# Performance work log

Measured on AMD Instinct MI355X. Metric: run time of the kernel, lower is better.

The kernel has to match this reference:

```python
import jax, jax.numpy as jnp
import numpy as np

B, TP, TF = 256, 128, 64
COV, D, OUT, CTRL, H, L = 64, 64, 32, 128, 512, 2


def _gru_layer(x, Wih, Whh, bih, bhh):
    # x: [B, T, in]; torch GRU gate order: r, z, n
    xg = jnp.einsum('bti,gi->btg', x, Wih) + bih  # [B, T, 3H]
    h0 = jnp.zeros((x.shape[0], Whh.shape[1]), x.dtype)

    def step(h, xg_t):
        gh = h @ Whh.T + bhh
        xr, xz, xn = jnp.split(xg_t, 3, axis=-1)
        hr, hz, hn = jnp.split(gh, 3, axis=-1)
        r = jax.nn.sigmoid(xr + hr)
        z = jax.nn.sigmoid(xz + hz)
        n = jnp.tanh(xn + r * hn)
        h = (1.0 - z) * n + z * h
        return h, h

    _, hs = jax.lax.scan(step, h0, jnp.swapaxes(xg, 0, 1))
    return jnp.swapaxes(hs, 0, 1)  # [B, T, H]


def setup_inputs() -> dict:
    key = jax.random.key(0)
    ks = jax.random.split(key, 32)
    s = 0.05
    inp = {
        'past_input': jax.random.normal(ks[0], (B, TP, COV), jnp.float32),
        'past_label': jax.random.normal(ks[1], (B, TP, OUT), jnp.float32),
        'future_input': jax.random.normal(ks[2], (B, TF, COV), jnp.float32),
        'gru_Wih_0': s * jax.random.normal(ks[3], (3 * H, COV), jnp.float32),
        'gru_Whh_0': s * jax.random.normal(ks[4], (3 * H, H), jnp.float32),
        'gru_bih_0': s * jax.random.normal(ks[5], (3 * H,), jnp.float32),
        'gru_bhh_0': s * jax.random.normal(ks[6], (3 * H,), jnp.float32),
        'gru_Wih_1': s * jax.random.normal(ks[7], (3 * H, H), jnp.float32),
        'gru_Whh_1': s * jax.random.normal(ks[8], (3 * H, H), jnp.float32),
        'gru_bih_1': s * jax.random.normal(ks[9], (3 * H,), jnp.float32),
        'gru_bhh_1': s * jax.random.normal(ks[10], (3 * H,), jnp.float32),
        'flow_u': s * jax.random.normal(ks[11], (D,), jnp.float32),
        'flow_w': s * jax.random.normal(ks[12], (D,), jnp.float32),
        'flow_b': s * jax.random.normal(ks[13], (D,), jnp.float32),
        'feat_W': s * jax.random.normal(ks[14], (D, H), jnp.float32),
        'feat_b': s * jax.random.normal(ks[15], (D,), jnp.float32),
        'ctrl_W1': s * jax.random.normal(ks[16], (CTRL, OUT), jnp.float32),
        'ctrl_b1': s * jax.random.normal(ks[17], (CTRL,), jnp.float32),
        'ctrl_W2': s * jax.random.normal(ks[18], (2 * D, CTRL), jnp.float32),
        'ctrl_b2': s * jax.random.normal(ks[19], (2 * D,), jnp.float32),
        'ctrlmu_W': s * jax.random.normal(ks[20], (D, D), jnp.float32),
        'ctrlmu_b': s * jax.random.normal(ks[21], (D,), jnp.float32),
        'out_W': s * jax.random.normal(ks[22], (OUT, D), jnp.float32),
        'out_b': s * jax.random.normal(ks[23], (OUT,), jnp.float32),
    }
    return inp


def reference(past_input, past_label, future_input,
              gru_Wih_0, gru_Whh_0, gru_bih_0, gru_bhh_0,
              gru_Wih_1, gru_Whh_1, gru_bih_1, gru_bhh_1,
              flow_u, flow_w, flow_b, feat_W, feat_b,
              ctrl_W1, ctrl_b1, ctrl_W2, ctrl_b2,
              ctrlmu_W, ctrlmu_b, out_W, out_b):
    cov = jnp.concatenate([past_input, future_input], axis=1)  # [B, T, COV]
    h1 = _gru_layer(cov, gru_Wih_0, gru_Whh_0, gru_bih_0, gru_bhh_0)
    cov_feat = _gru_layer(h1, gru_Wih_1, gru_Whh_1, gru_bih_1, gru_bhh_1)  # [B, T, H]
    Tp = past_input.shape[1]
    bsz = past_input.shape[0]

    def trans(mu_past, var_past, cov_t):
        # per-dim PlanarFlow vectorized over transition_dim
        a = jnp.tanh(flow_w * mu_past + flow_b)
        mu_prior = flow_u * a + cov_t @ feat_W.T + feat_b + mu_past
        coef = flow_u * flow_w * (1.0 - a * a)
        var_prior = 2.0 * coef * var_past + var_past + 1.0
        return mu_prior, var_prior

    def control(ctrl_in, mu_prior):
        hdn = jnp.tanh(ctrl_in @ ctrl_W1.T + ctrl_b1)
        cm, cls = jnp.split(hdn @ ctrl_W2.T + ctrl_b2, 2, axis=-1)
        cm = cm - (mu_prior @ ctrlmu_W.T + ctrlmu_b)
        return cm, jax.nn.softplus(cls)

    def fuse(mu_pr, var_pr, mu_po, var_po):
        s = var_po + var_pr
        mu_w = (var_po / s) * mu_pr + (var_pr / s) * mu_po
        return mu_w, var_pr * var_po / s

    def past_step(carry, xs):
        mu_post, var_post = carry
        cov_t, lab_t = xs
        mu_pr, var_pr = trans(mu_post, var_post, cov_t)
        pred = mu_pr @ out_W.T + out_b
        cm, cs = control(lab_t, mu_pr)
        return fuse(mu_pr, var_pr, cm, cs), (pred, cm, cs)

    def fut_step(carry, cov_t):
        mu_post, var_post = carry
        mu_pr, var_pr = trans(mu_post, var_post, cov_t)
        pred = mu_pr @ out_W.T + out_b
        cm, cs = control(pred, mu_pr)
        return fuse(mu_pr, var_pr, cm, cs), (pred, cm, cs)

    init = (jnp.zeros((bsz, D), cov.dtype), jnp.ones((bsz, D), cov.dtype))
    cov_p = jnp.swapaxes(cov_feat[:, :Tp], 0, 1)
    lab_p = jnp.swapaxes(past_label, 0, 1)
    carry, (pp, cmp_, csp) = jax.lax.scan(past_step, init, (cov_p, lab_p))
    cov_f = jnp.swapaxes(cov_feat[:, Tp:], 0, 1)
    _, (pf, cmf, csf) = jax.lax.scan(fut_step, carry, cov_f)

    pred = jnp.swapaxes(jnp.concatenate([pp, pf], axis=0), 0, 1)        # [B, T, OUT]
    cm = jnp.swapaxes(jnp.concatenate([cmp_, cmf], axis=0), 0, 1)[:, 1:]  # [B, T-1, D]
    cs = jnp.swapaxes(jnp.concatenate([csp, csf], axis=0), 0, 1)[:, 1:]   # [B, T-1, D]
    return pred, cm, cs
```

## Files before the change

### kernel.cpp

```cpp
#include <hip/hip_runtime.h>
#include <stdint.h>

#define DEV static __device__ __forceinline__

using short8 = __attribute__((ext_vector_type(8))) short;
using f32x4  = __attribute__((ext_vector_type(4))) float;
using gbl_u32 = const __attribute__((address_space(1))) unsigned int;
using lds_u32 = __attribute__((address_space(3))) unsigned int;

DEV float bf2f(short s) {
  unsigned u = ((unsigned)(unsigned short)s) << 16;
  float f; __builtin_memcpy(&f, &u, 4); return f;
}
DEV short f2bf(float f) {
  unsigned u; __builtin_memcpy(&u, &f, 4);
  u = (u + 0x7fffu + ((u >> 16) & 1u)) >> 16;
  return (short)u;
}
DEV void gload_lds16(const void* g, void* l) {
  __builtin_amdgcn_global_load_lds((gbl_u32*)g, (lds_u32*)l, 16, 0, 0);
}
DEV float sigm(float x) { return 1.f / (1.f + __expf(-x)); }
DEV float tanh_f(float x) {
  float e = __expf(2.f * x);
  return 1.f - 2.f * __builtin_amdgcn_rcpf(e + 1.f);
}
DEV unsigned load_agent(const unsigned int* p) {
  return __hip_atomic_load(p, __ATOMIC_RELAXED, __HIP_MEMORY_SCOPE_AGENT);
}
DEV void bar() {
  asm volatile("s_waitcnt lgkmcnt(0)" ::: "memory");
  __builtin_amdgcn_sched_barrier(0);
  __builtin_amdgcn_s_barrier();
  __builtin_amdgcn_sched_barrier(0);
}

__global__ void pack_covf_k(const float* __restrict__ past, const float* __restrict__ fut,
                            short* __restrict__ covf) {
  const int n = 192 * 16 * 2 * 512;
  for (int i = blockIdx.x * blockDim.x + threadIdx.x; i < n; i += gridDim.x * blockDim.x) {
    int e = i & 7, l = (i >> 3) & 63, kf = (i >> 9) & 1, g = (i >> 10) & 15, t = i >> 14;
    int b = g * 16 + (l & 15);
    int col = kf * 32 + (l >> 4) * 8 + e;
    float v = (t < 128) ? past[((size_t)b * 128 + t) * 64 + col]
                        : fut[((size_t)b * 64 + (t - 128)) * 64 + col];
    covf[i] = f2bf(v);
  }
}

__global__ void pack_lab_k(const float* __restrict__ lab, short* __restrict__ labp) {
  const int n = 128 * 256 * 32;
  for (int i = blockIdx.x * blockDim.x + threadIdx.x; i < n; i += gridDim.x * blockDim.x) {
    int c = i & 31, r = i >> 5;
    int b = r & 255, t = r >> 8;
    labp[i] = f2bf(lab[((size_t)b * 128 + t) * 32 + c]);
  }
}

DEV int gru_srcrow(int pr) {
  int j = pr / 96, w = pr % 96;
  return ((w >> 5) << 9) + j * 32 + (w & 31);
}

__global__ void pack_gru_k(const float* __restrict__ Wih, const float* __restrict__ Whh,
                           const float* __restrict__ bih, const float* __restrict__ bhh,
                           int Kin, short* __restrict__ Wihp, short* __restrict__ Whhp,
                           float* __restrict__ bihp, float* __restrict__ bhhp) {
  const int nW1 = 1536 * Kin, nW2 = 1536 * 512;
  const int total = nW1 + nW2 + 3072;
  for (int idx = blockIdx.x * blockDim.x + threadIdx.x; idx < total; idx += gridDim.x * blockDim.x) {
    if (idx < nW1) {
      int pr = idx / Kin, k = idx - pr * Kin;
      Wihp[idx] = f2bf(Wih[(size_t)gru_srcrow(pr) * Kin + k]);
    } else if (idx < nW1 + nW2) {
      int ii = idx - nW1;
      int j = ii / 49152, r = ii - j * 49152;
      int i = r & 7, slot = r >> 3;
      int l = slot & 63, sf = slot >> 6;
      int kqg = sf / 6, tile = sf - kqg * 6;
      int w = tile * 16 + (l & 15);
      int k = kqg * 32 + (l >> 4) * 8 + i;
      int srow = (w >> 5) * 512 + j * 32 + (w & 31);
      Whhp[ii] = f2bf(Whh[(size_t)srow * 512 + k]);
    } else if (idx < nW1 + nW2 + 1536) {
      int pr = idx - nW1 - nW2;
      bihp[pr] = bih[gru_srcrow(pr)];
    } else {
      int pr = idx - nW1 - nW2 - 1536;
      bhhp[pr] = bhh[gru_srcrow(pr)];
    }
  }
}

__global__ void pack_wih0f_k(const float* __restrict__ Wih0, short* __restrict__ wf) {
  const int n = 16 * 6 * 2 * 512;
  for (int i = blockIdx.x * blockDim.x + threadIdx.x; i < n; i += gridDim.x * blockDim.x) {
    int j = i / 6144, r = i - j * 6144;
    int tile = r >> 10, kf = (r >> 9) & 1, l = (r >> 3) & 63, e = r & 7;
    int srow = gru_srcrow(j * 96 + tile * 16 + (l & 15));
    int k = kf * 32 + (l >> 4) * 8 + e;
    wf[i] = f2bf(Wih0[(size_t)srow * 64 + k]);
  }
}

__global__ void pack_misc_k(const float* __restrict__ fw, const float* __restrict__ w1,
                            const float* __restrict__ w2, short* __restrict__ fwb,
                            short* __restrict__ w1b, short* __restrict__ w2b) {
  const int n1 = 64 * 512, n2 = 128 * 32, n3 = 128 * 128;
  const int total = n1 + n2 + n3;
  for (int i = blockIdx.x * blockDim.x + threadIdx.x; i < total; i += gridDim.x * blockDim.x) {
    if (i < n1) fwb[i] = f2bf(fw[i]);
    else if (i < n1 + n2) w1b[i - n1] = f2bf(w1[i - n1]);
    else w2b[i - n1 - n2] = f2bf(w2[i - n1 - n2]);
  }
}

__global__ void pack_vae_k(const float* __restrict__ outW, const float* __restrict__ cmuW,
                           const float* __restrict__ W1, const float* __restrict__ W2,
                           short* __restrict__ vwf) {
  const int n = 52 * 512;
  for (int i = blockIdx.x * blockDim.x + threadIdx.x; i < n; i += gridDim.x * blockDim.x) {
    int fr = i >> 9, l = (i >> 3) & 63, e = i & 7;
    int lm = l & 15, lh = l >> 4;
    float v;
    if (fr < 4) { int kt = fr >> 1, nt = fr & 1; v = outW[(nt * 16 + lm) * 64 + kt * 32 + lh * 8 + e]; }
    else if (fr < 12) { int f = fr - 4, kt = f >> 2, nt = f & 3; v = cmuW[(nt * 16 + lm) * 64 + kt * 32 + lh * 8 + e]; }
    else if (fr < 20) { int nt = fr - 12; v = W1[(nt * 16 + lm) * 32 + lh * 8 + e]; }
    else { int f = fr - 20, kt = f >> 3, nt = f & 7; v = W2[(nt * 16 + lm) * 128 + kt * 32 + lh * 8 + e]; }
    vwf[i] = f2bf(v);
  }
}

template <int BK, bool OBF16, bool DOTANH, bool AFRAG, int CMODE = 0>
__global__ __launch_bounds__(256) void gemm_bt_k(
    const short* __restrict__ A, const short* __restrict__ Bw,
    const float* __restrict__ bias, void* __restrict__ Cout,
    int M, int N, int K) {
  constexpr int BM = 128, BN = 128;
  __shared__ short As[BM * BK];
  __shared__ short Bs[BN * BK];
  const int tid = threadIdx.x, lane = tid & 63;
  const int wave = tid >> 6, wm = wave >> 1, wn = wave & 1;
  const int bm = blockIdx.x, bn = blockIdx.y;
  const int lm = lane & 15, lk = (lane >> 4) * 8;
  f32x4 acc[4][4] = {};
  for (int k0 = 0; k0 < K; k0 += BK) {
    constexpr int BYTES = BM * BK * 2;
#pragma unroll
    for (int it = 0; it < BYTES / 4096; ++it) {
      int o = it * 4096 + tid * 16;
      if (AFRAG) {
        int sub = o >> 10, gl = sub >> 1, kk2 = sub & 1, inb = o & 1023;
        size_t region = ((size_t)(bm >> 1) * 16 + (bm & 1) * 8 + gl) * 16 + (k0 >> 5) + kk2;
        gload_lds16((const char*)A + region * 1024 + inb, (char*)As + (o - lane * 16));
      } else {
        int row = o / (BK * 2);
        int col = o - row * (BK * 2);
        const char* srcA = (const char*)A + (((size_t)(bm * BM + row)) * K + k0) * 2 + col;
        gload_lds16(srcA, (char*)As + (o - lane * 16));
      }
      int row = o / (BK * 2);
      int col = o - row * (BK * 2);
      int rb = bn * BN + row;
      if (rb >= N) rb = N - 1;
      const char* srcB = (const char*)Bw + (((size_t)rb) * K + k0) * 2 + col;
      gload_lds16(srcB, (char*)Bs + (o - lane * 16));
    }
    __syncthreads();
#pragma unroll
    for (int kk = 0; kk < BK / 32; ++kk) {
      short8 av[4], bv[4];
#pragma unroll
      for (int i = 0; i < 4; ++i) {
        if (AFRAG)
          av[i] = *(const short8*)((const char*)As + (((wm * 4 + i) * 2 + kk) << 10) + lane * 16);
        else
          av[i] = *(const short8*)((const char*)As + ((wm * 64 + i * 16 + lm) * BK + kk * 32 + lk) * 2);
      }
#pragma unroll
      for (int jv = 0; jv < 4; ++jv)
        bv[jv] = *(const short8*)((const char*)Bs + ((wn * 64 + jv * 16 + lm) * BK + kk * 32 + lk) * 2);
#pragma unroll
      for (int i = 0; i < 4; ++i)
#pragma unroll
        for (int jv = 0; jv < 4; ++jv)
          acc[i][jv] = __builtin_amdgcn_mfma_f32_16x16x32_bf16(av[i], bv[jv], acc[i][jv], 0, 0, 0);
    }
    __syncthreads();
  }
  if (CMODE == 1) {
    const int NT = N >> 4;
#pragma unroll
    for (int jv = 0; jv < 4; ++jv) {
      int col = bn * BN + wn * 64 + jv * 16 + lm;
      if (col >= N) continue;
      float bvl = bias[col];
#pragma unroll
      for (int i = 0; i < 4; ++i) {
        int rowblk = bm * 8 + wm * 4 + i;
        f32x4 v = acc[i][jv];
        v[0] += bvl; v[1] += bvl; v[2] += bvl; v[3] += bvl;
        *(f32x4*)((float*)Cout + (((size_t)rowblk * NT + (col >> 4)) << 8) + lane * 4) = v;
      }
    }
  } else {
#pragma unroll
    for (int jv = 0; jv < 4; ++jv) {
      int col = bn * BN + wn * 64 + jv * 16 + lm;
      if (col >= N) continue;
      float bvl = bias[col];
#pragma unroll
      for (int i = 0; i < 4; ++i) {
        int row0 = bm * BM + wm * 64 + i * 16 + (lane >> 4) * 4;
#pragma unroll
        for (int r = 0; r < 4; ++r) {
          float v = acc[i][jv][r] + bvl;
          if (DOTANH) v = tanhf(v);
          size_t off = (size_t)(row0 + r) * N + col;
          if (OBF16) ((short*)Cout)[off] = f2bf(v);
          else ((float*)Cout)[off] = v;
        }
      }
    }
  }
}

template <int XGF>
__global__ __launch_bounds__(256) void gru_scan_k(
    const short* __restrict__ xg,
    const short* __restrict__ covf,
    const short* __restrict__ wihf_g,
    const short* __restrict__ Whhp,
    const float* __restrict__ bihp,
    const float* __restrict__ bhhp,
    short* __restrict__ hbuf,
    unsigned int* __restrict__ flags,
    int t0, int nsteps) {
  __shared__ short Wl[96 * 512];
  __shared__ short hs[16 * 512];
  __shared__ float sc[2][16 * 101];
  __shared__ float scx[2][16 * 33];
  __shared__ float bhs[96];
  __shared__ float bihn[32];
  const int tid = threadIdx.x, lane = tid & 63, wave = tid >> 6;
  const int x = blockIdx.x;
  const int g = (x & 7) + ((x >> 7) << 3);
  const int j = (x >> 3) & 15;
  unsigned int* __restrict__ myflags = flags + g * 16;
  unsigned int* __restrict__ hbuf32 = (unsigned int*)hbuf;
  {
    const char* wsrc = (const char*)Whhp + (size_t)j * 98304;
#pragma unroll 4
    for (int it = 0; it < 24; ++it) {
      int o = it * 4096 + tid * 16;
      gload_lds16(wsrc + o, (char*)Wl + (o - lane * 16));
    }
    if (tid < 96) {
      float b = bhhp[j * 96 + tid];
      if (XGF && tid < 64) b += bihp[j * 96 + tid];
      bhs[tid] = b;
    }
    if (XGF && tid < 32) bihn[tid] = bihp[j * 96 + 64 + tid];
  }
  const int wk = wave >> 1, wn3 = wave & 1;
  const int m = tid >> 4, up = tid & 15, u0 = up * 2;
  short8 wihf0{}, wihf1{}, wihf2{};
  if (XGF) {
    wihf0 = *(const short8*)(wihf_g + ((size_t)(j * 6 + wn3 * 3 + 0) * 2 + wk) * 512 + lane * 8);
    wihf1 = *(const short8*)(wihf_g + ((size_t)(j * 6 + wn3 * 3 + 1) * 2 + wk) * 512 + lane * 8);
    wihf2 = *(const short8*)(wihf_g + ((size_t)(j * 6 + wn3 * 3 + 2) * 2 + wk) * 512 + lane * 8);
  }
  for (int tl = 0; tl < nsteps; ++tl) {
    const int t = t0 + tl;
    if (tl > 0) {
      const unsigned tgt = (unsigned)tl;
      if (tid < 16) {
        const unsigned int* fp = myflags + tid;
        int guard = 0;
        while (load_agent(fp) < tgt && ++guard < 400000) {}
      }
    }
    __syncthreads();
    const char* hsrc = (const char*)hbuf + ((size_t)t * 16 + g) * 16384;
#pragma unroll
    for (int it = 0; it < 4; ++it) {
      int o = it * 4096 + tid * 16;
      gload_lds16(hsrc + o, (char*)hs + (o - lane * 16));
    }
    short8 cf{};
    unsigned int xr2 = 0, xz2 = 0, xn2 = 0;
    if (XGF) {
      cf = *(const short8*)(covf + (((size_t)t * 16 + g) * 2 + wk) * 512 + lane * 8);
    } else {
      const unsigned int* xp = (const unsigned int*)(xg + ((size_t)tl * 256 + g * 16 + m) * 1536 + j * 96);
      xr2 = xp[up]; xz2 = xp[16 + up]; xn2 = xp[32 + up];
    }
    __syncthreads();
    f32x4 a3[3] = {};
    f32x4 ax0 = {0.f, 0.f, 0.f, 0.f}, ax1 = {0.f, 0.f, 0.f, 0.f};
#pragma unroll
    for (int kq = 0; kq < 8; ++kq) {
      int kqg = wk * 8 + kq;
      short8 av = *(const short8*)((const char*)hs + (kqg << 10) + lane * 16);
#pragma unroll
      for (int n = 0; n < 3; ++n) {
        short8 bv = *(const short8*)((const char*)Wl + ((kqg * 6 + wn3 * 3 + n) << 10) + lane * 16);
        a3[n] = __builtin_amdgcn_mfma_f32_16x16x32_bf16(av, bv, a3[n], 0, 0, 0);
      }
    }
    if (XGF) {
      a3[0] = __builtin_amdgcn_mfma_f32_16x16x32_bf16(cf, wihf0, a3[0], 0, 0, 0);
      if (wn3 == 0) {
        a3[1] = __builtin_amdgcn_mfma_f32_16x16x32_bf16(cf, wihf1, a3[1], 0, 0, 0);
        a3[2] = __builtin_amdgcn_mfma_f32_16x16x32_bf16(cf, wihf2, a3[2], 0, 0, 0);
      } else {
        ax0 = __builtin_amdgcn_mfma_f32_16x16x32_bf16(cf, wihf1, ax0, 0, 0, 0);
        ax1 = __builtin_amdgcn_mfma_f32_16x16x32_bf16(cf, wihf2, ax1, 0, 0, 0);
      }
    }
#pragma unroll
    for (int n = 0; n < 3; ++n)
#pragma unroll
      for (int rr = 0; rr < 4; ++rr)
        sc[wk][((lane >> 4) * 4 + rr) * 101 + (wn3 * 3 + n) * 16 + (lane & 15)] = a3[n][rr];
    if (XGF && wn3 == 1) {
#pragma unroll
      for (int rr = 0; rr < 4; ++rr) {
        scx[wk][((lane >> 4) * 4 + rr) * 33 + (lane & 15)] = ax0[rr];
        scx[wk][((lane >> 4) * 4 + rr) * 33 + 16 + (lane & 15)] = ax1[rr];
      }
    }
    __syncthreads();
    {
      float Sr0 = sc[0][m * 101 + u0] + sc[1][m * 101 + u0];
      float Sr1 = sc[0][m * 101 + u0 + 1] + sc[1][m * 101 + u0 + 1];
      float Sz0 = sc[0][m * 101 + 32 + u0] + sc[1][m * 101 + 32 + u0];
      float Sz1 = sc[0][m * 101 + 33 + u0] + sc[1][m * 101 + 33 + u0];
      float Sn0 = sc[0][m * 101 + 64 + u0] + sc[1][m * 101 + 64 + u0];
      float Sn1 = sc[0][m * 101 + 65 + u0] + sc[1][m * 101 + 65 + u0];
      int hpa = ((j * 64 + (up >> 2) * 16 + m) << 4) + ((u0 & 7) << 1);
      unsigned int hpu = *(const unsigned int*)((const char*)hs + hpa);
      float hp0 = bf2f((short)(hpu & 0xffff)), hp1 = bf2f((short)(hpu >> 16));
      float r0, r1, z0, z1, n0, n1;
      if (XGF) {
        float Sx0 = scx[0][m * 33 + u0] + scx[1][m * 33 + u0];
        float Sx1 = scx[0][m * 33 + u0 + 1] + scx[1][m * 33 + u0 + 1];
        r0 = sigm(Sr0 + bhs[u0]);
        r1 = sigm(Sr1 + bhs[u0 + 1]);
        z0 = sigm(Sz0 + bhs[32 + u0]);
        z1 = sigm(Sz1 + bhs[33 + u0]);
        n0 = tanhf(Sx0 + bihn[u0] + r0 * (Sn0 + bhs[64 + u0]));
        n1 = tanhf(Sx1 + bihn[u0 + 1] + r1 * (Sn1 + bhs[65 + u0]));
      } else {
        r0 = sigm(bf2f((short)(xr2 & 0xffff)) + Sr0 + bhs[u0]);
        r1 = sigm(bf2f((short)(xr2 >> 16)) + Sr1 + bhs[u0 + 1]);
        z0 = sigm(bf2f((short)(xz2 & 0xffff)) + Sz0 + bhs[32 + u0]);
        z1 = sigm(bf2f((short)(xz2 >> 16)) + Sz1 + bhs[33 + u0]);
        n0 = tanhf(bf2f((short)(xn2 & 0xffff)) + r0 * (Sn0 + bhs[64 + u0]));
        n1 = tanhf(bf2f((short)(xn2 >> 16)) + r1 * (Sn1 + bhs[65 + u0]));
      }
      float h0 = (1.f - z0) * n0 + z0 * hp0;
      float h1 = (1.f - z1) * n1 + z1 * hp1;
      unsigned int hv = (unsigned int)(unsigned short)f2bf(h0) |
                        ((unsigned int)(unsigned short)f2bf(h1) << 16);
      size_t oi = ((size_t)(t + 1) * 16 + g) * 4096 +
                  (j * 64 + (up >> 2) * 16 + m) * 4 + (up & 3);
      __hip_atomic_store(hbuf32 + oi, hv, __ATOMIC_RELAXED, __HIP_MEMORY_SCOPE_AGENT);
    }
    __syncthreads();
    if (tid == 0)
      __hip_atomic_store(myflags + j, (unsigned)(tl + 1),
                         __ATOMIC_RELAXED, __HIP_MEMORY_SCOPE_AGENT);
    __syncthreads();
  }
}

#define PAST_STEP(T, FN, CMR, CSR)                                           \
  do {                                                                       \
    f32x4 muPr, varPr;                                                       \
    _Pragma("unroll") for (int r = 0; r < 4; ++r) {                          \
      float m_ = muC[r];                                                     \
      float a_ = tanh_f(fw1 * m_ + fb1);                                     \
      muPr[r] = fu1 * a_ + FN[r] + m_;                                       \
      float cf_ = fu1 * fw1 * (1.f - a_ * a_);                               \
      varPr[r] = 2.f * cf_ * varC[r] + varC[r] + 1.f;                        \
    }                                                                        \
    f32x4 cmNow = CMR, csNow = CSR;                                          \
    FN = *(const f32x4*)(feat_img + (((size_t)((T) + 2) * 16 + bg) * 4 + w) * 256 + l * 4); \
    if ((T) + 2 < 128) {                                                     \
      CMR = *(const f32x4*)(ctrl_img + (((size_t)((T) + 2) * 16 + bg) * 8 + w) * 256 + l * 4); \
      CSR = *(const f32x4*)(ctrl_img + (((size_t)((T) + 2) * 16 + bg) * 8 + 4 + w) * 256 + l * 4); \
    }                                                                        \
    _Pragma("unroll") for (int r = 0; r < 4; ++r) {                          \
      int row_ = m4 * 4 + r;                                                 \
      *(short*)((char*)muA + ((row_ * 128 + (w * 16 + c) * 2) ^ ((row_ & 7) << 4))) = f2bf(muPr[r]); \
    }                                                                        \
    bar();                                                                   \
    short8 muAf0 = *(const short8*)((const char*)muA + ((c * 128 + m4 * 16) ^ ((c & 7) << 4))); \
    short8 muAf1 = *(const short8*)((const char*)muA + ((c * 128 + 64 + m4 * 16) ^ ((c & 7) << 4))); \
    if (w == 0) *(short8*)(muprb + (((size_t)(T) * 16 + bg) * 2) * 512 + l * 8) = muAf0; \
    if (w == 1) *(short8*)(muprb + (((size_t)(T) * 16 + bg) * 2 + 1) * 512 + l * 8) = muAf1; \
    f32x4 mcC = {0.f, 0.f, 0.f, 0.f};                                        \
    mcC = __builtin_amdgcn_mfma_f32_16x16x32_bf16(muAf0, cmuf0, mcC, 0, 0, 0); \
    mcC = __builtin_amdgcn_mfma_f32_16x16x32_bf16(muAf1, cmuf1, mcC, 0, 0, 0); \
    bar();                                                                   \
    _Pragma("unroll") for (int r = 0; r < 4; ++r) {                          \
      float vp_ = varPr[r], mp_ = muPr[r];                                   \
      float cmv_ = cmNow[r] - (mcC[r] + cmub1);                              \
      float x_ = csNow[r];                                                   \
      float cs_ = (x_ > 20.f) ? x_ : __logf(1.f + __expf(x_));               \
      if ((T) >= 1) {                                                        \
        size_t b_ = (size_t)(bg * 16 + m4 * 4 + r);                          \
        out[1572864 + b_ * 12224 + (size_t)((T) - 1) * 64 + w * 16 + c] = cmv_; \
        out[4702208 + b_ * 12224 + (size_t)((T) - 1) * 64 + w * 16 + c] = cs_;  \
      }                                                                      \
      float s_ = cs_ + vp_;                                                  \
      float rs_ = __builtin_amdgcn_rcpf(s_);                                 \
      muC[r] = cs_ * rs_ * mp_ + vp_ * rs_ * cmv_;                           \
      varC[r] = vp_ * cs_ * rs_;                                             \
    }                                                                        \
  } while (0)

#define FUT_STEP(T, FN)                                                      \
  do {                                                                       \
    f32x4 muPr, varPr;                                                       \
    _Pragma("unroll") for (int r = 0; r < 4; ++r) {                          \
      float m_ = muC[r];                                                     \
      float a_ = tanh_f(fw1 * m_ + fb1);                                     \
      muPr[r] = fu1 * a_ + FN[r] + m_;                                       \
      float cf_ = fu1 * fw1 * (1.f - a_ * a_);                               \
      varPr[r] = 2.f * cf_ * varC[r] + varC[r] + 1.f;                        \
    }                                                                        \
    if ((T) + 2 < 192)                                                       \
      FN = *(const f32x4*)(feat_img + (((size_t)((T) + 2) * 16 + bg) * 4 + w) * 256 + l * 4); \
    _Pragma("unroll") for (int r = 0; r < 4; ++r) {                          \
      int row_ = m4 * 4 + r;                                                 \
      *(short*)((char*)muA + ((row_ * 128 + (w * 16 + c) * 2) ^ ((row_ & 7) << 4))) = f2bf(muPr[r]); \
    }                                                                        \
    bar();                                                                   \
    short8 muAf0 = *(const short8*)((const char*)muA + ((c * 128 + m4 * 16) ^ ((c & 7) << 4))); \
    short8 muAf1 = *(const short8*)((const char*)muA + ((c * 128 + 64 + m4 * 16) ^ ((c & 7) << 4))); \
    f32x4 mcC = {0.f, 0.f, 0.f, 0.f};                                        \
    mcC = __builtin_amdgcn_mfma_f32_16x16x32_bf16(muAf0, cmuf0, mcC, 0, 0, 0); \
    mcC = __builtin_amdgcn_mfma_f32_16x16x32_bf16(muAf1, cmuf1, mcC, 0, 0, 0); \
    if (w < 2) {                                                             \
      f32x4 predC = {0.f, 0.f, 0.f, 0.f};                                    \
      predC = __builtin_amdgcn_mfma_f32_16x16x32_bf16(muAf0, outWf0, predC, 0, 0, 0); \
      predC = __builtin_amdgcn_mfma_f32_16x16x32_bf16(muAf1, outWf1, predC, 0, 0, 0); \
      _Pragma("unroll") for (int r = 0; r < 4; ++r) {                        \
        float pv_ = predC[r] + outb1;                                        \
        out[(size_t)(bg * 16 + m4 * 4 + r) * 6144 + (T) * 32 + w * 16 + c] = pv_; \
        int row_ = m4 * 4 + r;                                               \
        *(short*)((char*)predA + ((row_ * 64 + (w * 16 + c) * 2) ^ ((row_ & 3) << 4))) = f2bf(pv_); \
      }                                                                      \
    }                                                                        \
    bar();                                                                   \
    short8 pAf = *(const short8*)((const char*)predA + ((c * 64 + m4 * 16) ^ ((c & 3) << 4))); \
    f32x4 z0 = {0.f, 0.f, 0.f, 0.f}, z1 = {0.f, 0.f, 0.f, 0.f};              \
    z0 = __builtin_amdgcn_mfma_f32_16x16x32_bf16(pAf, *(const short8*)((const char*)Wctl + (2 * w) * 1024 + l * 16), z0, 0, 0, 0); \
    z1 = __builtin_amdgcn_mfma_f32_16x16x32_bf16(pAf, *(const short8*)((const char*)Wctl + (2 * w + 1) * 1024 + l * 16), z1, 0, 0, 0); \
    _Pragma("unroll") for (int r = 0; r < 4; ++r) {                          \
      int row_ = m4 * 4 + r;                                                 \
      *(short*)((char*)hdnA + ((row_ * 256 + ((2 * w) * 16 + c) * 2) ^ ((row_ & 7) << 4))) = f2bf(tanh_f(z0[r] + b1a)); \
      *(short*)((char*)hdnA + ((row_ * 256 + ((2 * w + 1) * 16 + c) * 2) ^ ((row_ & 7) << 4))) = f2bf(tanh_f(z1[r] + b1b)); \
    }                                                                        \
    bar();                                                                   \
    short8 hAf0 = *(const short8*)((const char*)hdnA + ((c * 256 + 0 * 64 + m4 * 16) ^ ((c & 7) << 4))); \
    short8 hAf1 = *(const short8*)((const char*)hdnA + ((c * 256 + 1 * 64 + m4 * 16) ^ ((c & 7) << 4))); \
    short8 hAf2 = *(const short8*)((const char*)hdnA + ((c * 256 + 2 * 64 + m4 * 16) ^ ((c & 7) << 4))); \
    short8 hAf3 = *(const short8*)((const char*)hdnA + ((c * 256 + 3 * 64 + m4 * 16) ^ ((c & 7) << 4))); \
    f32x4 zcm = {0.f, 0.f, 0.f, 0.f}, zcs = {0.f, 0.f, 0.f, 0.f};            \
    zcm = __builtin_amdgcn_mfma_f32_16x16x32_bf16(hAf0, *(const short8*)((const char*)Wctl + (8 + 0 * 8 + w) * 1024 + l * 16), zcm, 0, 0, 0); \
    zcm = __builtin_amdgcn_mfma_f32_16x16x32_bf16(hAf1, *(const short8*)((const char*)Wctl + (8 + 1 * 8 + w) * 1024 + l * 16), zcm, 0, 0, 0); \
    zcm = __builtin_amdgcn_mfma_f32_16x16x32_bf16(hAf2, *(const short8*)((const char*)Wctl + (8 + 2 * 8 + w) * 1024 + l * 16), zcm, 0, 0, 0); \
    zcm = __builtin_amdgcn_mfma_f32_16x16x32_bf16(hAf3, *(const short8*)((const char*)Wctl + (8 + 3 * 8 + w) * 1024 + l * 16), zcm, 0, 0, 0); \
    zcs = __builtin_amdgcn_mfma_f32_16x16x32_bf16(hAf0, *(const short8*)((const char*)Wctl + (8 + 0 * 8 + 4 + w) * 1024 + l * 16), zcs, 0, 0, 0); \
    zcs = __builtin_amdgcn_mfma_f32_16x16x32_bf16(hAf1, *(const short8*)((const char*)Wctl + (8 + 1 * 8 + 4 + w) * 1024 + l * 16), zcs, 0, 0, 0); \
    zcs = __builtin_amdgcn_mfma_f32_16x16x32_bf16(hAf2, *(const short8*)((const char*)Wctl + (8 + 2 * 8 + 4 + w) * 1024 + l * 16), zcs, 0, 0, 0); \
    zcs = __builtin_amdgcn_mfma_f32_16x16x32_bf16(hAf3, *(const short8*)((const char*)Wctl + (8 + 3 * 8 + 4 + w) * 1024 + l * 16), zcs, 0, 0, 0); \
    bar();                                                                   \
    _Pragma("unroll") for (int r = 0; r < 4; ++r) {                          \
      float vp_ = varPr[r], mp_ = muPr[r];                                   \
      float cmv_ = (zcm[r] + b2cm) - (mcC[r] + cmub1);                       \
      float x_ = zcs[r] + b2cs;                                              \
      float cs_ = (x_ > 20.f) ? x_ : __logf(1.f + __expf(x_));               \
      size_t b_ = (size_t)(bg * 16 + m4 * 4 + r);                            \
      out[1572864 + b_ * 12224 + (size_t)((T) - 1) * 64 + w * 16 + c] = cmv_; \
      out[4702208 + b_ * 12224 + (size_t)((T) - 1) * 64 + w * 16 + c] = cs_;  \
      float s_ = cs_ + vp_;                                                  \
      float rs_ = __builtin_amdgcn_rcpf(s_);                                 \
      muC[r] = cs_ * rs_ * mp_ + vp_ * rs_ * cmv_;                           \
      varC[r] = vp_ * cs_ * rs_;                                             \
    }                                                                        \
  } while (0)

__global__ __launch_bounds__(256) void vae_k(
    const float* __restrict__ feat_img, const float* __restrict__ ctrl_img,
    const short* __restrict__ vwf,
    const float* __restrict__ flow_u, const float* __restrict__ flow_w,
    const float* __restrict__ flow_b, const float* __restrict__ outb,
    const float* __restrict__ b1, const float* __restrict__ b2,
    const float* __restrict__ cmub, short* __restrict__ muprb,
    float* __restrict__ out) {
  __shared__ short Wctl[40 * 512];
  __shared__ short muA[16 * 64];
  __shared__ short predA[16 * 32];
  __shared__ short hdnA[16 * 128];
  const int tid = threadIdx.x, l = tid & 63, w = tid >> 6;
  const int m4 = l >> 4, c = l & 15, bg = blockIdx.x;
  {
    const char* src = (const char*)vwf + 12288;
#pragma unroll
    for (int it = 0; it < 10; ++it) {
      int o = it * 4096 + tid * 16;
      gload_lds16(src + o, (char*)Wctl + (o - l * 16));
    }
  }
  short8 cmuf0 = *(const short8*)(vwf + (4 + w) * 512 + l * 8);
  short8 cmuf1 = *(const short8*)(vwf + (8 + w) * 512 + l * 8);
  short8 outWf0 = *(const short8*)(vwf + ((w & 1)) * 512 + l * 8);
  short8 outWf1 = *(const short8*)(vwf + (2 + (w & 1)) * 512 + l * 8);
  float fw1 = flow_w[w * 16 + c], fu1 = flow_u[w * 16 + c];
  float fb1 = flow_b[w * 16 + c], cmub1 = cmub[w * 16 + c];
  float outb1 = outb[(w & 1) * 16 + c];
  float b1a = b1[(2 * w) * 16 + c], b1b = b1[(2 * w + 1) * 16 + c];
  float b2cm = b2[w * 16 + c], b2cs = b2[(4 + w) * 16 + c];
  f32x4 muC = {0.f, 0.f, 0.f, 0.f}, varC = {1.f, 1.f, 1.f, 1.f};
  f32x4 fN0 = *(const f32x4*)(feat_img + ((size_t)bg * 4 + w) * 256 + l * 4);
  f32x4 fN1 = *(const f32x4*)(feat_img + ((size_t)(16 + bg) * 4 + w) * 256 + l * 4);
  f32x4 cmA = *(const f32x4*)(ctrl_img + ((size_t)bg * 8 + w) * 256 + l * 4);
  f32x4 csA = *(const f32x4*)(ctrl_img + ((size_t)bg * 8 + 4 + w) * 256 + l * 4);
  f32x4 cmB = *(const f32x4*)(ctrl_img + ((size_t)(16 + bg) * 8 + w) * 256 + l * 4);
  f32x4 csB = *(const f32x4*)(ctrl_img + ((size_t)(16 + bg) * 8 + 4 + w) * 256 + l * 4);
  __syncthreads();
  for (int t2 = 0; t2 < 128; t2 += 2) {
    PAST_STEP(t2, fN0, cmA, csA);
    PAST_STEP(t2 + 1, fN1, cmB, csB);
  }
  asm volatile("s_waitcnt vmcnt(0)" ::: "memory");
  __builtin_amdgcn_sched_barrier(0);
  __builtin_amdgcn_s_barrier();
  for (int t2 = 128; t2 < 192; t2 += 2) {
    FUT_STEP(t2, fN0);
    FUT_STEP(t2 + 1, fN1);
  }
}

__global__ __launch_bounds__(512) void pred_past_k(
    const short* __restrict__ muprb, const short* __restrict__ vwf,
    const float* __restrict__ outb, float* __restrict__ out) {
  const int l = threadIdx.x & 63;
  const int w = blockIdx.x * 8 + (threadIdx.x >> 6);
  const int t = w >> 4, bg = w & 15;
  const int m4 = l >> 4, c = l & 15;
  short8 a0 = *(const short8*)(muprb + ((size_t)w * 2 + 0) * 512 + l * 8);
  short8 a1 = *(const short8*)(muprb + ((size_t)w * 2 + 1) * 512 + l * 8);
  float outb2[2] = {outb[c], outb[16 + c]};
#pragma unroll
  for (int nt = 0; nt < 2; ++nt) {
    short8 w0 = *(const short8*)(vwf + (0 * 2 + nt) * 512 + l * 8);
    short8 w1 = *(const short8*)(vwf + (1 * 2 + nt) * 512 + l * 8);
    f32x4 p = {0.f, 0.f, 0.f, 0.f};
    p = __builtin_amdgcn_mfma_f32_16x16x32_bf16(a0, w0, p, 0, 0, 0);
    p = __builtin_amdgcn_mfma_f32_16x16x32_bf16(a1, w1, p, 0, 0, 0);
#pragma unroll
    for (int r = 0; r < 4; ++r)
      out[(size_t)(bg * 16 + m4 * 4 + r) * 6144 + t * 32 + nt * 16 + c] = p[r] + outb2[nt];
  }
}

extern "C" void kernel_launch(void* const* d_in, const int* in_sizes, int n_in,
                              void* d_out, int out_size, void* d_ws, size_t ws_size,
                              hipStream_t stream) {
  (void)in_sizes; (void)n_in; (void)out_size; (void)ws_size;
  const float* past_input = (const float*)d_in[0];
  const float* past_label = (const float*)d_in[1];
  const float* future_input = (const float*)d_in[2];
  const float* Wih0 = (const float*)d_in[3];
  const float* Whh0 = (const float*)d_in[4];
  const float* bih0 = (const float*)d_in[5];
  const float* bhh0 = (const float*)d_in[6];
  const float* Wih1 = (const float*)d_in[7];
  const float* Whh1 = (const float*)d_in[8];
  const float* bih1 = (const float*)d_in[9];
  const float* bhh1 = (const float*)d_in[10];
  const float* flow_u = (const float*)d_in[11];
  const float* flow_w = (const float*)d_in[12];
  const float* flow_b = (const float*)d_in[13];
  const float* feat_W = (const float*)d_in[14];
  const float* feat_b = (const float*)d_in[15];
  const float* ctrl_W1 = (const float*)d_in[16];
  const float* ctrl_b1 = (const float*)d_in[17];
  const float* ctrl_W2 = (const float*)d_in[18];
  const float* ctrl_b2 = (const float*)d_in[19];
  const float* cmuW = (const float*)d_in[20];
  const float* cmub = (const float*)d_in[21];
  const float* outW = (const float*)d_in[22];
  const float* outb = (const float*)d_in[23];

  char* ws = (char*)d_ws;
  size_t off = 0;
  auto alloc = [&](size_t bytes) -> char* {
    char* p = ws + off;
    off += (bytes + 255) & ~(size_t)255;
    return p;
  };
  short* covf  = (short*)alloc(192ull * 16 * 2 * 512 * 2);
  short* labp  = (short*)alloc(32768ull * 32 * 2);
  short* Wih0p = (short*)alloc(1536ull * 64 * 2);
  short* Whh0p = (short*)alloc(1536ull * 512 * 2);
  short* Wih1p = (short*)alloc(1536ull * 512 * 2);
  short* Whh1p = (short*)alloc(1536ull * 512 * 2);
  float* bih0p = (float*)alloc(1536 * 4);
  float* bhh0p = (float*)alloc(1536 * 4);
  float* bih1p = (float*)alloc(1536 * 4);
  float* bhh1p = (float*)alloc(1536 * 4);
  short* featWb = (short*)alloc(64ull * 512 * 2);
  short* W1b   = (short*)alloc(128ull * 32 * 2);
  short* W2b   = (short*)alloc(128ull * 128 * 2);
  short* vwf   = (short*)alloc(52ull * 512 * 2);
  short* wih0f = (short*)alloc(16ull * 6 * 2 * 512 * 2);
  short* xgc   = (short*)alloc(48ull * 256 * 1536 * 2);
  short* h1buf = (short*)alloc(193ull * 256 * 512 * 2);
  short* cfbuf = (short*)alloc(193ull * 256 * 512 * 2);
  unsigned int* flg = (unsigned int*)alloc(8 * 16 * 16 * 4);
  float* feat_img = (float*)xgc;
  short* hdnb     = (short*)((char*)xgc + 12582912);
  float* ctrl_img = (float*)((char*)xgc + 20971520);
  short* muprb    = (short*)covf;

  hipMemsetAsync(flg, 0, 8 * 16 * 16 * 4, stream);
  hipMemsetAsync(h1buf, 0, 256 * 512 * 2, stream);
  hipMemsetAsync(cfbuf, 0, 256 * 512 * 2, stream);

  pack_covf_k<<<2048, 256, 0, stream>>>(past_input, future_input, covf);
  pack_lab_k<<<1024, 256, 0, stream>>>(past_label, labp);
  pack_gru_k<<<1024, 256, 0, stream>>>(Wih0, Whh0, bih0, bhh0, 64, Wih0p, Whh0p, bih0p, bhh0p);
  pack_gru_k<<<1024, 256, 0, stream>>>(Wih1, Whh1, bih1, bhh1, 512, Wih1p, Whh1p, bih1p, bhh1p);
  pack_wih0f_k<<<96, 256, 0, stream>>>(Wih0, wih0f);
  pack_misc_k<<<64, 256, 0, stream>>>(feat_W, ctrl_W1, ctrl_W2, featWb, W1b, W2b);
  pack_vae_k<<<104, 256, 0, stream>>>(outW, cmuW, ctrl_W1, ctrl_W2, vwf);

  gru_scan_k<1><<<256, 256, 0, stream>>>(
      nullptr, covf, wih0f, Whh0p, bih0p, bhh0p, h1buf, flg, 0, 192);
  for (int c = 0; c < 4; ++c) {
    gemm_bt_k<64, true, false, true><<<dim3(96, 12), 256, 0, stream>>>(
        h1buf + (size_t)(1 + c * 48) * 131072, Wih1p, bih1p, xgc, 12288, 1536, 512);
    gru_scan_k<0><<<256, 256, 0, stream>>>(
        xgc, nullptr, nullptr, Whh1p, nullptr, bhh1p, cfbuf,
        flg + (1 + c) * 256, c * 48, 48);
  }
  gemm_bt_k<64, false, false, true, 1><<<dim3(384, 1), 256, 0, stream>>>(
      cfbuf + 131072, featWb, feat_b, feat_img, 49152, 64, 512);
  gemm_bt_k<32, true, true, false><<<dim3(256, 1), 256, 0, stream>>>(
      labp, W1b, ctrl_b1, hdnb, 32768, 128, 32);
  gemm_bt_k<64, false, false, false, 1><<<dim3(256, 1), 256, 0, stream>>>(
      hdnb, W2b, ctrl_b2, ctrl_img, 32768, 128, 128);

  vae_k<<<16, 256, 0, stream>>>(feat_img, ctrl_img, vwf, flow_u, flow_w, flow_b,
                                outb, ctrl_b1, ctrl_b2, cmub, muprb, (float*)d_out);
  pred_past_k<<<256, 512, 0, stream>>>(muprb, vwf, outb, (float*)d_out);
}
```

Measured before the change: 1.369 ms.

## Replace per-block flags with tagged value pairs for GRU cross-block sync

Instead of writing h to global memory and then bumping a per-block flag behind two barriers, each thread atomically stores a 64-bit word that packs the timestep tag with its bf16 pair of h values, into a double-buffered exchange area. Consumers poll the tags, then read the h values straight from the pair buffer into LDS. This removes the trailing barriers and the flag round trip from the serial critical path of the recurrence. In exchange it doubles the bytes exchanged per step, adds polling loops over 16 words per thread, and keeps a separate plain store to hbuf for later stages.

```diff
diff --git a/kernel.cpp b/kernel.cpp
--- a/kernel.cpp
+++ b/kernel.cpp
@@ -25,7 +25,7 @@
   float e = __expf(2.f * x);
   return 1.f - 2.f * __builtin_amdgcn_rcpf(e + 1.f);
 }
-DEV unsigned load_agent(const unsigned int* p) {
+DEV unsigned long long load_pair(const unsigned long long* p) {
   return __hip_atomic_load(p, __ATOMIC_RELAXED, __HIP_MEMORY_SCOPE_AGENT);
 }
 DEV void bar() {
@@ -234,7 +234,7 @@
     const float* __restrict__ bihp,
     const float* __restrict__ bhhp,
     short* __restrict__ hbuf,
-    unsigned int* __restrict__ flags,
+    unsigned long long* __restrict__ pairs,
     int t0, int nsteps) {
   __shared__ short Wl[96 * 512];
   __shared__ short hs[16 * 512];
@@ -246,8 +246,8 @@
   const int x = blockIdx.x;
   const int g = (x & 7) + ((x >> 7) << 3);
   const int j = (x >> 3) & 15;
-  unsigned int* __restrict__ myflags = flags + g * 16;
   unsigned int* __restrict__ hbuf32 = (unsigned int*)hbuf;
+  unsigned int* __restrict__ hs32 = (unsigned int*)hs;
   {
     const char* wsrc = (const char*)Whhp + (size_t)j * 98304;
 #pragma unroll 4
@@ -264,6 +264,7 @@
   }
   const int wk = wave >> 1, wn3 = wave & 1;
   const int m = tid >> 4, up = tid & 15, u0 = up * 2;
+  const int pidx = j * 256 + (up >> 2) * 64 + m * 4 + (up & 3);
   short8 wihf0{}, wihf1{}, wihf2{};
   if (XGF) {
     wihf0 = *(const short8*)(wihf_g + ((size_t)(j * 6 + wn3 * 3 + 0) * 2 + wk) * 512 + lane * 8);
@@ -272,20 +273,33 @@
   }
   for (int tl = 0; tl < nsteps; ++tl) {
     const int t = t0 + tl;
-    if (tl > 0) {
-      const unsigned tgt = (unsigned)tl;
-      if (tid < 16) {
-        const unsigned int* fp = myflags + tid;
-        int guard = 0;
-        while (load_agent(fp) < tgt && ++guard < 400000) {}
-      }
+    const unsigned long long* pb = pairs + (((size_t)(t & 1) * 16 + g) << 12);
+    if (tid < 16) {
+      int guard = 0;
+      while ((unsigned)(load_pair(pb + tid * 256) >> 32) != (unsigned)t &&
+             ++guard < 400000) {}
     }
     __syncthreads();
-    const char* hsrc = (const char*)hbuf + ((size_t)t * 16 + g) * 16384;
-#pragma unroll
-    for (int it = 0; it < 4; ++it) {
-      int o = it * 4096 + tid * 16;
-      gload_lds16(hsrc + o, (char*)hs + (o - lane * 16));
+    {
+      unsigned int hvv[16];
+      int guard = 0;
+      for (;;) {
+        unsigned long long pr[16];
+#pragma unroll
+        for (int k = 0; k < 16; ++k)
+          pr[k] = load_pair(pb + tid + k * 256);
+        bool ok = true;
+#pragma unroll
+        for (int k = 0; k < 16; ++k)
+          ok &= ((unsigned)(pr[k] >> 32) == (unsigned)t);
+        if (ok || ++guard >= 20000) {
+#pragma unroll
+          for (int k = 0; k < 16; ++k) hvv[k] = (unsigned)pr[k];
+          break;
+        }
+      }
+#pragma unroll
+      for (int k = 0; k < 16; ++k) hs32[tid + k * 256] = hvv[k];
     }
     short8 cf{};
     unsigned int xr2 = 0, xz2 = 0, xn2 = 0;
@@ -363,15 +377,11 @@
       float h1 = (1.f - z1) * n1 + z1 * hp1;
       unsigned int hv = (unsigned int)(unsigned short)f2bf(h0) |
                         ((unsigned int)(unsigned short)f2bf(h1) << 16);
-      size_t oi = ((size_t)(t + 1) * 16 + g) * 4096 +
-                  (j * 64 + (up >> 2) * 16 + m) * 4 + (up & 3);
-      __hip_atomic_store(hbuf32 + oi, hv, __ATOMIC_RELAXED, __HIP_MEMORY_SCOPE_AGENT);
-    }
-    __syncthreads();
-    if (tid == 0)
-      __hip_atomic_store(myflags + j, (unsigned)(tl + 1),
-                         __ATOMIC_RELAXED, __HIP_MEMORY_SCOPE_AGENT);
-    __syncthreads();
+      unsigned long long pv = ((unsigned long long)(unsigned)(t + 1) << 32) | hv;
+      __hip_atomic_store(pairs + (((size_t)((t + 1) & 1) * 16 + g) << 12) + pidx,
+                         pv, __ATOMIC_RELAXED, __HIP_MEMORY_SCOPE_AGENT);
+      hbuf32[((size_t)(t + 1) * 16 + g) * 4096 + pidx] = hv;
+    }
   }
 }
 
@@ -623,13 +633,17 @@
   short* xgc   = (short*)alloc(48ull * 256 * 1536 * 2);
   short* h1buf = (short*)alloc(193ull * 256 * 512 * 2);
   short* cfbuf = (short*)alloc(193ull * 256 * 512 * 2);
-  unsigned int* flg = (unsigned int*)alloc(8 * 16 * 16 * 4);
+  unsigned long long* hpair = (unsigned long long*)alloc(2ull * 16 * 4096 * 8);
+  unsigned long long* cpair = (unsigned long long*)alloc(2ull * 16 * 4096 * 8);
   float* feat_img = (float*)xgc;
   short* hdnb     = (short*)((char*)xgc + 12582912);
   float* ctrl_img = (float*)((char*)xgc + 20971520);
   short* muprb    = (short*)covf;
 
-  hipMemsetAsync(flg, 0, 8 * 16 * 16 * 4, stream);
+  hipMemsetAsync(hpair, 0, 16 * 4096 * 8, stream);
+  hipMemsetAsync(cpair, 0, 16 * 4096 * 8, stream);
+  hipMemsetAsync(hpair + 16 * 4096, 0xFF, 16 * 4096 * 8, stream);
+  hipMemsetAsync(cpair + 16 * 4096, 0xFF, 16 * 4096 * 8, stream);
   hipMemsetAsync(h1buf, 0, 256 * 512 * 2, stream);
   hipMemsetAsync(cfbuf, 0, 256 * 512 * 2, stream);
 
@@ -642,13 +656,12 @@
   pack_vae_k<<<104, 256, 0, stream>>>(outW, cmuW, ctrl_W1, ctrl_W2, vwf);
 
   gru_scan_k<1><<<256, 256, 0, stream>>>(
-      nullptr, covf, wih0f, Whh0p, bih0p, bhh0p, h1buf, flg, 0, 192);
+      nullptr, covf, wih0f, Whh0p, bih0p, bhh0p, h1buf, hpair, 0, 192);
   for (int c = 0; c < 4; ++c) {
     gemm_bt_k<64, true, false, true><<<dim3(96, 12), 256, 0, stream>>>(
         h1buf + (size_t)(1 + c * 48) * 131072, Wih1p, bih1p, xgc, 12288, 1536, 512);
     gru_scan_k<0><<<256, 256, 0, stream>>>(
-        xgc, nullptr, nullptr, Whh1p, nullptr, bhh1p, cfbuf,
-        flg + (1 + c) * 256, c * 48, 48);
+        xgc, nullptr, nullptr, Whh1p, nullptr, bhh1p, cfbuf, cpair, c * 48, 48);
   }
   gemm_bt_k<64, false, false, true, 1><<<dim3(384, 1), 256, 0, stream>>>(
       cfbuf + 131072, featWb, feat_b, feat_img, 49152, 64, 512);
```

Measured after the change: 1.568 ms. 14.6% more time.
